# Kernel optimization log

Hardware: AMD Instinct MI355X
Metric: run time of the kernel (lower is better)

## Reference

```python
import jax, jax.numpy as jnp
import numpy as np

N_NODES = 200_000
N_EDGES = 6_400_000
N_GRAPHS = 512


def _graph_conv(x, src, dst, W_rel, b_rel, W_root, n_nodes):
    # PyG GraphConv (aggr='add'): lin_rel(sum_{j->i} x_j) + lin_root(x_i)
    agg = jax.ops.segment_sum(x[src], dst, num_segments=n_nodes)  # [N, in]
    return agg @ W_rel.T + b_rel + x @ W_root.T


def setup_inputs() -> dict:
    key = jax.random.key(0)
    ks = jax.random.split(key, 12)
    x = jax.random.normal(ks[0], (N_NODES, 3), dtype=jnp.float32)
    edge_index = jax.random.randint(ks[1], (2, N_EDGES), 0, N_NODES, dtype=jnp.int64)
    batch = jnp.sort(jax.random.randint(ks[2], (N_NODES,), 0, N_GRAPHS, dtype=jnp.int64))

    def xavier(k, shape):
        fan_out, fan_in = shape
        lim = np.sqrt(6.0 / (fan_in + fan_out)).astype(np.float32)
        return jax.random.uniform(k, shape, jnp.float32, -lim, lim)

    return {
        "x": x, "edge_index": edge_index, "batch": batch,
        "W1_rel": xavier(ks[3], (32, 3)),  "b1": jnp.zeros((32,), jnp.float32), "W1_root": xavier(ks[4], (32, 3)),
        "W2_rel": xavier(ks[5], (16, 32)), "b2": jnp.zeros((16,), jnp.float32), "W2_root": xavier(ks[6], (16, 32)),
        "W3_rel": xavier(ks[7], (8, 16)),  "b3": jnp.zeros((8,), jnp.float32),  "W3_root": xavier(ks[8], (8, 16)),
        "W_lin": xavier(ks[9], (1, 8)),    "b_lin": jnp.zeros((1,), jnp.float32),
    }


def reference(x, edge_index, batch,
              W1_rel, b1, W1_root,
              W2_rel, b2, W2_root,
              W3_rel, b3, W3_root,
              W_lin, b_lin):
    src, dst = edge_index[0], edge_index[1]
    h = jax.nn.relu(_graph_conv(x, src, dst, W1_rel, b1, W1_root, N_NODES))
    h = jax.nn.relu(_graph_conv(h, src, dst, W2_rel, b2, W2_root, N_NODES))
    h = jax.nn.relu(_graph_conv(h, src, dst, W3_rel, b3, W3_root, N_NODES))
    pooled = jax.ops.segment_max(h, batch, num_segments=N_GRAPHS)  # [G, 8]
    out = pooled @ W_lin.T + b_lin  # [G, 1]
    return out[:, 0]
```

## Files before the change

### kernel.cpp

```cpp
#include <hip/hip_runtime.h>
#include <hip/hip_fp16.h>

#define N_NODES 200000
#define N_EDGES 6400000
#define N_GRAPHS 512

#define NB 3125
#define CHUNK 8192
#define NCH 782
#define NGRP 25
#define CPG 32
#define SEG 13
#define SCAP 3072

typedef float vf4 __attribute__((ext_vector_type(4)));
typedef float vf2 __attribute__((ext_vector_type(2)));
typedef unsigned vu2 __attribute__((ext_vector_type(2)));

__device__ __forceinline__ unsigned ntload_u(const unsigned* p) {
  return __builtin_nontemporal_load(p);
}
__device__ __forceinline__ int ntload_i(const int* p) { return __builtin_nontemporal_load(p); }
__device__ __forceinline__ float ntload_f(const float* p) {
  return __builtin_nontemporal_load(p);
}
__device__ __forceinline__ float2 ntload_f2(const float* p) {
  vf2 v = __builtin_nontemporal_load((const vf2*)p);
  return make_float2(v.x, v.y);
}
__device__ __forceinline__ void ntstore_u2(unsigned* p, uint2 v) {
  vu2 t = {v.x, v.y};
  __builtin_nontemporal_store(t, (vu2*)p);
}
__device__ __forceinline__ void ntstore_f2(float* p, float2 v) {
  vf2 t = {v.x, v.y};
  __builtin_nontemporal_store(t, (vf2*)p);
}
__device__ __forceinline__ void ntstore_f4(float* p, float4 v) {
  vf4 t = {v.x, v.y, v.z, v.w};
  __builtin_nontemporal_store(t, (vf4*)p);
}
__device__ __forceinline__ void ntstore_u(unsigned* p, unsigned v) {
  __builtin_nontemporal_store(v, p);
}


__global__ __launch_bounds__(256) void count_kernel(const int* __restrict__ dst,
                                                    unsigned short* __restrict__ H) {
  __shared__ unsigned hist[NB];
  for (int i = threadIdx.x; i < NB; i += 256) hist[i] = 0;
  __syncthreads();
  int c = blockIdx.x;
  long e0 = (long)c * CHUNK;
  long rem = (long)N_EDGES - e0;
  int n = rem > CHUNK ? CHUNK : (int)rem;
  for (int i = threadIdx.x; i < n; i += 256) atomicAdd(&hist[dst[e0 + i] >> 6], 1u);
  __syncthreads();
  for (int i = threadIdx.x; i < NB; i += 256) H[(size_t)c * NB + i] = (unsigned short)hist[i];
}

__global__ __launch_bounds__(256) void scan_bins1_kernel(unsigned short* __restrict__ H,
                                                         unsigned* __restrict__ P) {
  int b = blockIdx.x * 256 + threadIdx.x;
  int g = blockIdx.y;
  if (b >= NB) return;
  int c0 = g * CPG, c1 = min(NCH, (g + 1) * CPG);
  unsigned run = 0;
  for (int c = c0; c < c1; c++) {
    unsigned t = H[(size_t)c * NB + b];
    H[(size_t)c * NB + b] = (unsigned short)run;
    run += t;
  }
  P[(size_t)g * NB + b] = run;
}

__global__ __launch_bounds__(256) void scan_bins2_kernel(unsigned* __restrict__ P,
                                                         unsigned* __restrict__ bucketTotal) {
  int b = blockIdx.x * 256 + threadIdx.x;
  if (b >= NB) return;
  unsigned run = 0;
  for (int g = 0; g < NGRP; g++) {
    unsigned t = P[(size_t)g * NB + b];
    P[(size_t)g * NB + b] = run;
    run += t;
  }
  bucketTotal[b] = run;
}

__global__ __launch_bounds__(256) void scan_total_kernel(const unsigned* __restrict__ bucketTotal,
                                                         unsigned* __restrict__ bucketStart) {
  __shared__ unsigned sv[256 * SEG];
  __shared__ unsigned partial[256];
  int t = threadIdx.x;
  for (int i = t; i < 256 * SEG; i += 256) sv[i] = (i < NB) ? bucketTotal[i] : 0u;
  __syncthreads();
  unsigned sum = 0;
#pragma unroll
  for (int k = 0; k < SEG; k++) sum += sv[t * SEG + k];
  partial[t] = sum;
  __syncthreads();
  for (int off = 1; off < 256; off <<= 1) {
    unsigned add = (t >= off) ? partial[t - off] : 0u;
    __syncthreads();
    partial[t] += add;
    __syncthreads();
  }
  unsigned run = partial[t] - sum;
#pragma unroll
  for (int k = 0; k < SEG; k++) {
    unsigned w = sv[t * SEG + k];
    sv[t * SEG + k] = run;
    run += w;
  }
  __syncthreads();
  for (int i = t; i < NB; i += 256) bucketStart[i] = sv[i];
  if (t == 0) bucketStart[NB] = N_EDGES;
}

__global__ __launch_bounds__(256) void scatter_sorted_kernel(
    const int* __restrict__ src, const int* __restrict__ dst,
    const unsigned short* __restrict__ H, const unsigned* __restrict__ P,
    const unsigned* __restrict__ bucketStart, unsigned* __restrict__ packed) {
  __shared__ unsigned ssort[CHUNK];
  __shared__ unsigned short sbort[CHUNK];
  __shared__ unsigned hist[3328];
  __shared__ unsigned cur[3328];
  __shared__ unsigned partial[256];
  int t = threadIdx.x;
  int c = blockIdx.x;
  int g = c / CPG;
  long e0 = (long)c * CHUNK;
  long rem = (long)N_EDGES - e0;
  int n = rem > CHUNK ? CHUNK : (int)rem;
  for (int i = t; i < 3328; i += 256) hist[i] = 0;
  __syncthreads();
  for (int i = t; i < n; i += 256) atomicAdd(&hist[dst[e0 + i] >> 6], 1u);
  __syncthreads();
  unsigned a[SEG], sum = 0;
#pragma unroll
  for (int k = 0; k < SEG; k++) { a[k] = hist[SEG * t + k]; sum += a[k]; }
  partial[t] = sum;
  __syncthreads();
  for (int off = 1; off < 256; off <<= 1) {
    unsigned add = (t >= off) ? partial[t - off] : 0u;
    __syncthreads();
    partial[t] += add;
    __syncthreads();
  }
  unsigned run = partial[t] - sum;
#pragma unroll
  for (int k = 0; k < SEG; k++) {
    hist[SEG * t + k] = run;
    cur[SEG * t + k] = run;
    run += a[k];
  }
  __syncthreads();
  for (int i = t; i < n; i += 256) {
    int d = dst[e0 + i], s = src[e0 + i];
    int b = d >> 6;
    unsigned r = atomicAdd(&cur[b], 1u);
    ssort[r] = ((unsigned)s << 7) | (unsigned)(d & 63);
    sbort[r] = (unsigned short)b;
  }
  __syncthreads();
  for (int b = t; b < NB; b += 256)
    cur[b] = bucketStart[b] + P[(size_t)g * NB + b] + H[(size_t)c * NB + b] - hist[b];
  __syncthreads();
  for (int j = t; j < n; j += 256) packed[cur[sbort[j]] + j] = ssort[j];
}

__global__ __launch_bounds__(256) void sort2_kernel(const unsigned* __restrict__ packedA,
                                                    const unsigned* __restrict__ bucketStart,
                                                    unsigned* __restrict__ packedB,
                                                    unsigned* __restrict__ nodeStart) {
  __shared__ unsigned buf[SCAP];
  __shared__ unsigned buf2[SCAP];
  __shared__ unsigned hist[64], base[64], cur[64];
  int t = threadIdx.x, b = blockIdx.x;
  unsigned s0 = bucketStart[b], s1 = bucketStart[b + 1];
  int n = (int)(s1 - s0);
  if (t < 64) hist[t] = 0;
  for (int i = t; i < n; i += 256) buf[i] = packedA[s0 + i];
  __syncthreads();
  for (int i = t; i < n; i += 256) atomicAdd(&hist[buf[i] & 63u], 1u);
  __syncthreads();
  if (t == 0) {
    unsigned run = 0;
    for (int k = 0; k < 64; k++) {
      unsigned v = hist[k];
      base[k] = run;
      cur[k] = run;
      run += v;
    }
  }
  __syncthreads();
  if (t < 64) nodeStart[b * 64 + t] = s0 + base[t];
  for (int i = t; i < n; i += 256) {
    unsigned p = buf[i];
    unsigned pos = atomicAdd(&cur[p & 63u], 1u);
    buf2[pos] = p >> 7;
  }
  __syncthreads();
  for (int i = t; i < n; i += 256) packedB[s0 + i] = buf2[i];
  if (b == NB - 1 && t == 0) nodeStart[N_NODES] = N_EDGES;
}

__global__ __launch_bounds__(256) void xpad_kernel(const float* __restrict__ x,
                                                   float4* __restrict__ xp) {
  int n = blockIdx.x * 256 + threadIdx.x;
  if (n >= N_NODES) return;
  xp[n] = make_float4(x[3 * n], x[3 * n + 1], x[3 * n + 2], 0.f);
}

__device__ __forceinline__ void half8_unpack(uint4 g, float* f) {
  const __half2* h2 = reinterpret_cast<const __half2*>(&g);
#pragma unroll
  for (int j = 0; j < 4; j++) {
    float2 fj = __half22float2(h2[j]);
    f[2 * j] = fj.x;
    f[2 * j + 1] = fj.y;
  }
}

__global__ __launch_bounds__(256) void layer1_kernel(
    const unsigned* __restrict__ packed, const unsigned* __restrict__ nodeStart,
    const float4* __restrict__ xp,
    const float* __restrict__ W1_rel, const float* __restrict__ b1,
    const float* __restrict__ W1_root,
    const float* __restrict__ W2_rel, const float* __restrict__ W2_root,
    unsigned* __restrict__ t2h, float* __restrict__ r2) {
  __shared__ float sW1rel[96], sW1root[96], sb1[32], sW2rel[512], sW2root[512];
  __shared__ float plds[256 * 4];
  for (int i = threadIdx.x; i < 96; i += 256) { sW1rel[i] = W1_rel[i]; sW1root[i] = W1_root[i]; }
  for (int i = threadIdx.x; i < 32; i += 256) sb1[i] = b1[i];
  for (int i = threadIdx.x; i < 512; i += 256) { sW2rel[i] = W2_rel[i]; sW2root[i] = W2_root[i]; }
  __syncthreads();
  int t = threadIdx.x, ln = t >> 2, part = t & 3;
  int node = blockIdx.x * 64 + ln;
  unsigned s1v = ntload_u(&nodeStart[node + 1]);
  float a0 = 0.f, a1 = 0.f, a2 = 0.f;
  for (unsigned base = ntload_u(&nodeStart[node]) + part; base < s1v; base += 16) {
    unsigned i1 = base + 4, i2 = base + 8, i3 = base + 12;
    unsigned e0 = ntload_u(&packed[base]);
    unsigned e1 = ntload_u(&packed[i1]);
    unsigned e2 = ntload_u(&packed[i2]);
    unsigned e3 = ntload_u(&packed[i3]);
    float4 g0 = xp[e0], g1 = xp[e1], g2 = xp[e2], g3 = xp[e3];
    float m1 = (i1 < s1v) ? 1.f : 0.f;
    float m2 = (i2 < s1v) ? 1.f : 0.f;
    float m3 = (i3 < s1v) ? 1.f : 0.f;
    a0 += g0.x + m1 * g1.x + m2 * g2.x + m3 * g3.x;
    a1 += g0.y + m1 * g1.y + m2 * g2.y + m3 * g3.y;
    a2 += g0.z + m1 * g1.z + m2 * g2.z + m3 * g3.z;
  }
  plds[t * 4] = a0; plds[t * 4 + 1] = a1; plds[t * 4 + 2] = a2;
  __syncthreads();
  int pb = ln * 16;
  float A0 = plds[pb] + plds[pb + 4] + plds[pb + 8] + plds[pb + 12];
  float A1 = plds[pb + 1] + plds[pb + 5] + plds[pb + 9] + plds[pb + 13];
  float A2 = plds[pb + 2] + plds[pb + 6] + plds[pb + 10] + plds[pb + 14];
  float4 xv = xp[node];
  float h[32];
#pragma unroll
  for (int k = 0; k < 32; k++) {
    float v = sW1rel[3 * k] * A0 + sW1rel[3 * k + 1] * A1 + sW1rel[3 * k + 2] * A2 +
              sW1root[3 * k] * xv.x + sW1root[3 * k + 1] * xv.y + sW1root[3 * k + 2] * xv.z +
              sb1[k];
    h[k] = fmaxf(v, 0.f);
  }
  int jb = part * 4;
  float tv[4], rv[4];
#pragma unroll
  for (int j = 0; j < 4; j++) {
    float acc = 0.f, accr = 0.f;
#pragma unroll
    for (int k = 0; k < 32; k++) {
      acc += sW2rel[32 * (jb + j) + k] * h[k];
      accr += sW2root[32 * (jb + j) + k] * h[k];
    }
    tv[j] = acc;
    rv[j] = accr;
  }
  __half2 p0 = __halves2half2(__float2half_rn(tv[0]), __float2half_rn(tv[1]));
  __half2 p1 = __halves2half2(__float2half_rn(tv[2]), __float2half_rn(tv[3]));
  ntstore_u2(&t2h[(size_t)node * 8 + part * 2], make_uint2(*(unsigned*)&p0, *(unsigned*)&p1));
  ntstore_f4(&r2[(size_t)node * 16 + jb], make_float4(rv[0], rv[1], rv[2], rv[3]));
}

__global__ __launch_bounds__(256) void layer2_kernel(
    const unsigned* __restrict__ packed, const unsigned* __restrict__ nodeStart,
    const uint4* __restrict__ t2h4, const float* __restrict__ r2,
    const float* __restrict__ b2,
    const float* __restrict__ W3_rel, const float* __restrict__ W3_root,
    unsigned* __restrict__ t3h, float* __restrict__ r3) {
  __shared__ float sW3rel[128], sW3root[128], sb2[16];
  __shared__ float plds[256 * 9];
  __shared__ float hlds[32 * 16];
  for (int i = threadIdx.x; i < 128; i += 256) { sW3rel[i] = W3_rel[i]; sW3root[i] = W3_root[i]; }
  if (threadIdx.x < 16) sb2[threadIdx.x] = b2[threadIdx.x];
  __syncthreads();
  int t = threadIdx.x, ln = t >> 3, p = t & 7;
  int node = blockIdx.x * 32 + ln;
  int half = p & 1;
  unsigned s1v = ntload_u(&nodeStart[node + 1]);
  float acc[8];
#pragma unroll
  for (int j = 0; j < 8; j++) acc[j] = 0.f;
  for (unsigned base = ntload_u(&nodeStart[node]) + (p >> 1); base < s1v; base += 16) {
    unsigned i1 = base + 4, i2 = base + 8, i3 = base + 12;
    unsigned e0 = ntload_u(&packed[base]);
    unsigned e1 = ntload_u(&packed[i1]);
    unsigned e2 = ntload_u(&packed[i2]);
    unsigned e3 = ntload_u(&packed[i3]);
    uint4 g0 = t2h4[(size_t)e0 * 2 + half];
    uint4 g1 = t2h4[(size_t)e1 * 2 + half];
    uint4 g2 = t2h4[(size_t)e2 * 2 + half];
    uint4 g3 = t2h4[(size_t)e3 * 2 + half];
    float m1 = (i1 < s1v) ? 1.f : 0.f;
    float m2 = (i2 < s1v) ? 1.f : 0.f;
    float m3 = (i3 < s1v) ? 1.f : 0.f;
    float f0[8], f1[8], f2[8], f3[8];
    half8_unpack(g0, f0);
    half8_unpack(g1, f1);
    half8_unpack(g2, f2);
    half8_unpack(g3, f3);
#pragma unroll
    for (int j = 0; j < 8; j++)
      acc[j] += f0[j] + m1 * f1[j] + m2 * f2[j] + m3 * f3[j];
  }
#pragma unroll
  for (int j = 0; j < 8; j++) plds[t * 9 + j] = acc[j];
  __syncthreads();
  {
    float2 rv = ntload_f2(&r2[(size_t)node * 16 + 2 * p]);
    float hv[2];
#pragma unroll
    for (int k2 = 0; k2 < 2; k2++) {
      int f = 2 * p + k2;
      int fh = f >> 3, fi = f & 7;
      int q0 = (ln * 8 + fh) * 9 + fi;
      float s = plds[q0] + plds[q0 + 18] + plds[q0 + 36] + plds[q0 + 54];
      hv[k2] = s + sb2[f] + (k2 == 0 ? rv.x : rv.y);
    }
    hlds[ln * 16 + 2 * p] = fmaxf(hv[0], 0.f);
    hlds[ln * 16 + 2 * p + 1] = fmaxf(hv[1], 0.f);
  }
  __syncthreads();
  const float* W = (p < 4) ? sW3rel : sW3root;
  int rbase = (p < 4) ? 2 * p : 2 * (p - 4);
  float o0 = 0.f, o1 = 0.f;
#pragma unroll
  for (int k = 0; k < 16; k++) {
    float hv = hlds[ln * 16 + k];
    o0 += W[16 * rbase + k] * hv;
    o1 += W[16 * (rbase + 1) + k] * hv;
  }
  if (p < 4) {
    __half2 pk = __halves2half2(__float2half_rn(o0), __float2half_rn(o1));
    ntstore_u(&t3h[(size_t)node * 4 + p], *(unsigned*)&pk);
  } else {
    ntstore_f2(&r3[(size_t)node * 8 + rbase], make_float2(o0, o1));
  }
}

__global__ __launch_bounds__(256) void layer3_kernel(
    const unsigned* __restrict__ packed, const unsigned* __restrict__ nodeStart,
    const uint4* __restrict__ t3h4, const float* __restrict__ r3,
    const float* __restrict__ b3,
    const int* __restrict__ batch, unsigned* __restrict__ pooled) {
  __shared__ float plds[256 * 9];
  __shared__ float sb3[8];
  __shared__ int sgid[32];
  if (threadIdx.x < 8) sb3[threadIdx.x] = b3[threadIdx.x];
  __syncthreads();
  int t = threadIdx.x, ln = t >> 3, p = t & 7;
  int node = blockIdx.x * 32 + ln;
  unsigned s1v = ntload_u(&nodeStart[node + 1]);
  float acc[8];
#pragma unroll
  for (int j = 0; j < 8; j++) acc[j] = 0.f;
  for (unsigned base = ntload_u(&nodeStart[node]) + p; base < s1v; base += 32) {
    unsigned i1 = base + 8, i2 = base + 16, i3 = base + 24;
    unsigned e0 = ntload_u(&packed[base]);
    unsigned e1 = ntload_u(&packed[i1]);
    unsigned e2 = ntload_u(&packed[i2]);
    unsigned e3 = ntload_u(&packed[i3]);
    uint4 g0 = t3h4[e0];
    uint4 g1 = t3h4[e1];
    uint4 g2 = t3h4[e2];
    uint4 g3 = t3h4[e3];
    float m1 = (i1 < s1v) ? 1.f : 0.f;
    float m2 = (i2 < s1v) ? 1.f : 0.f;
    float m3 = (i3 < s1v) ? 1.f : 0.f;
    float f0[8], f1[8], f2[8], f3[8];
    half8_unpack(g0, f0);
    half8_unpack(g1, f1);
    half8_unpack(g2, f2);
    half8_unpack(g3, f3);
#pragma unroll
    for (int j = 0; j < 8; j++)
      acc[j] += f0[j] + m1 * f1[j] + m2 * f2[j] + m3 * f3[j];
  }
#pragma unroll
  for (int j = 0; j < 8; j++) plds[t * 9 + j] = acc[j];
  __syncthreads();
  int gg = ntload_i(&batch[node]);
  int q0 = ln * 72 + p;
  float v = plds[q0] + plds[q0 + 9] + plds[q0 + 18] + plds[q0 + 27] +
            plds[q0 + 36] + plds[q0 + 45] + plds[q0 + 54] + plds[q0 + 63];
  float h = fmaxf(v + sb3[p] + ntload_f(&r3[(size_t)node * 8 + p]), 0.f);
  __syncthreads();
  plds[ln * 9 + p] = h;
  if (p == 0) sgid[ln] = gg;
  __syncthreads();
  if (t < 8) {
    int gcur = sgid[0];
    float m = plds[t];
    for (int l = 1; l < 32; l++) {
      int g2 = sgid[l];
      float hv = plds[l * 9 + t];
      if (g2 != gcur) {
        atomicMax(&pooled[8 * gcur + t], __float_as_uint(m));
        gcur = g2;
        m = hv;
      } else {
        m = fmaxf(m, hv);
      }
    }
    atomicMax(&pooled[8 * gcur + t], __float_as_uint(m));
  }
}

__global__ __launch_bounds__(256) void final_kernel(
    const unsigned* __restrict__ pooled, const float* __restrict__ W_lin,
    const float* __restrict__ b_lin, float* __restrict__ out) {
  int g = blockIdx.x * blockDim.x + threadIdx.x;
  if (g >= N_GRAPHS) return;
  float acc = b_lin[0];
#pragma unroll
  for (int f = 0; f < 8; f++) acc += __uint_as_float(pooled[8 * g + f]) * W_lin[f];
  out[g] = acc;
}

extern "C" void kernel_launch(void* const* d_in, const int* in_sizes, int n_in,
                              void* d_out, int out_size, void* d_ws, size_t ws_size,
                              hipStream_t stream) {
  const float* x = (const float*)d_in[0];
  const int* ei = (const int*)d_in[1];
  const int* src = ei;
  const int* dst = ei + N_EDGES;
  const int* batch = (const int*)d_in[2];
  const float* W1_rel = (const float*)d_in[3];
  const float* b1 = (const float*)d_in[4];
  const float* W1_root = (const float*)d_in[5];
  const float* W2_rel = (const float*)d_in[6];
  const float* b2 = (const float*)d_in[7];
  const float* W2_root = (const float*)d_in[8];
  const float* W3_rel = (const float*)d_in[9];
  const float* b3 = (const float*)d_in[10];
  const float* W3_root = (const float*)d_in[11];
  const float* W_lin = (const float*)d_in[12];
  const float* b_lin = (const float*)d_in[13];
  float* out = (float*)d_out;

  char* ws = (char*)d_ws;
  unsigned* packedA = (unsigned*)(ws + 0);
  float* r2 = (float*)(ws + 0);
  float* r3 = (float*)(ws + 12800000);
  unsigned* t3h = (unsigned*)(ws + 19200000);
  float4* xpad = (float4*)(ws + 22400000);
  unsigned short* H = (unsigned short*)(ws + 25600000);
  unsigned* packedB = (unsigned*)(ws + 25600000);
  unsigned* t2h = (unsigned*)(ws + 51200128);
  unsigned* pooled = (unsigned*)(ws + 57600128);
  unsigned* bucketStart = (unsigned*)(ws + 57616512);
  unsigned* bucketTotal = (unsigned*)(ws + 57629016);
  unsigned* P = (unsigned*)(ws + 57641516);
  unsigned* nodeStart = (unsigned*)(ws + 57954016);

  hipMemsetAsync(pooled, 0, N_GRAPHS * 8 * sizeof(unsigned), stream);
  hipMemsetAsync(packedB + N_EDGES, 0, 128, stream);

  count_kernel<<<NCH, 256, 0, stream>>>(dst, H);
  scan_bins1_kernel<<<dim3((NB + 255) / 256, NGRP), 256, 0, stream>>>(H, P);
  scan_bins2_kernel<<<(NB + 255) / 256, 256, 0, stream>>>(P, bucketTotal);
  scan_total_kernel<<<1, 256, 0, stream>>>(bucketTotal, bucketStart);
  scatter_sorted_kernel<<<NCH, 256, 0, stream>>>(src, dst, H, P, bucketStart, packedA);
  sort2_kernel<<<NB, 256, 0, stream>>>(packedA, bucketStart, packedB, nodeStart);
  xpad_kernel<<<(N_NODES + 255) / 256, 256, 0, stream>>>(x, xpad);

  layer1_kernel<<<NB, 256, 0, stream>>>(packedB, nodeStart, xpad,
                                        W1_rel, b1, W1_root, W2_rel, W2_root, t2h, r2);
  layer2_kernel<<<N_NODES / 32, 256, 0, stream>>>(packedB, nodeStart, (const uint4*)t2h, r2, b2,
                                                  W3_rel, W3_root, t3h, r3);
  layer3_kernel<<<N_NODES / 32, 256, 0, stream>>>(packedB, nodeStart, (const uint4*)t3h, r3, b3,
                                                  batch, pooled);
  final_kernel<<<(N_GRAPHS + 255) / 256, 256, 0, stream>>>(pooled, W_lin, b_lin, out);
}
```

Baseline: 430.8 us.

## Coarsen first-pass sort buckets to 1024 nodes with per-wave histograms

The two-pass counting sort of edges by destination now uses 196 coarse buckets of 1024 nodes instead of 3125 buckets of 64. This shrinks the histogram, prefix-scan and offset arrays, and the count and scatter kernels keep one privatized histogram per wavefront to cut LDS atomic contention. The second pass uses 512-thread blocks that sort each bucket straight from global memory into its final position. This trades the LDS staging for uncoalesced global scatter writes and far fewer blocks with longer per-block work.

```diff
diff --git a/kernel.cpp b/kernel.cpp
--- a/kernel.cpp
+++ b/kernel.cpp
@@ -5,13 +5,13 @@
 #define N_EDGES 6400000
 #define N_GRAPHS 512
 
-#define NB 3125
+#define NB1 196
+#define CB 1024
 #define CHUNK 8192
 #define NCH 782
 #define NGRP 25
 #define CPG 32
-#define SEG 13
-#define SCAP 3072
+#define ST2 512
 
 typedef float vf4 __attribute__((ext_vector_type(4)));
 typedef float vf2 __attribute__((ext_vector_type(2)));
@@ -47,41 +47,44 @@
 
 __global__ __launch_bounds__(256) void count_kernel(const int* __restrict__ dst,
                                                     unsigned short* __restrict__ H) {
-  __shared__ unsigned hist[NB];
-  for (int i = threadIdx.x; i < NB; i += 256) hist[i] = 0;
+  __shared__ unsigned hist[4][NB1];
+  int t = threadIdx.x, w = t >> 6;
+  for (int i = t; i < 4 * NB1; i += 256) ((unsigned*)hist)[i] = 0;
   __syncthreads();
   int c = blockIdx.x;
   long e0 = (long)c * CHUNK;
   long rem = (long)N_EDGES - e0;
   int n = rem > CHUNK ? CHUNK : (int)rem;
-  for (int i = threadIdx.x; i < n; i += 256) atomicAdd(&hist[dst[e0 + i] >> 6], 1u);
-  __syncthreads();
-  for (int i = threadIdx.x; i < NB; i += 256) H[(size_t)c * NB + i] = (unsigned short)hist[i];
+  for (int i = t; i < n; i += 256) atomicAdd(&hist[w][dst[e0 + i] >> 10], 1u);
+  __syncthreads();
+  for (int b = t; b < NB1; b += 256)
+    H[(size_t)c * NB1 + b] =
+        (unsigned short)(hist[0][b] + hist[1][b] + hist[2][b] + hist[3][b]);
 }
 
 __global__ __launch_bounds__(256) void scan_bins1_kernel(unsigned short* __restrict__ H,
                                                          unsigned* __restrict__ P) {
   int b = blockIdx.x * 256 + threadIdx.x;
   int g = blockIdx.y;
-  if (b >= NB) return;
+  if (b >= NB1) return;
   int c0 = g * CPG, c1 = min(NCH, (g + 1) * CPG);
   unsigned run = 0;
   for (int c = c0; c < c1; c++) {
-    unsigned t = H[(size_t)c * NB + b];
-    H[(size_t)c * NB + b] = (unsigned short)run;
+    unsigned t = H[(size_t)c * NB1 + b];
+    H[(size_t)c * NB1 + b] = (unsigned short)run;
     run += t;
   }
-  P[(size_t)g * NB + b] = run;
+  P[(size_t)g * NB1 + b] = run;
 }
 
 __global__ __launch_bounds__(256) void scan_bins2_kernel(unsigned* __restrict__ P,
                                                          unsigned* __restrict__ bucketTotal) {
   int b = blockIdx.x * 256 + threadIdx.x;
-  if (b >= NB) return;
+  if (b >= NB1) return;
   unsigned run = 0;
   for (int g = 0; g < NGRP; g++) {
-    unsigned t = P[(size_t)g * NB + b];
-    P[(size_t)g * NB + b] = run;
+    unsigned t = P[(size_t)g * NB1 + b];
+    P[(size_t)g * NB1 + b] = run;
     run += t;
   }
   bucketTotal[b] = run;
@@ -89,15 +92,10 @@
 
 __global__ __launch_bounds__(256) void scan_total_kernel(const unsigned* __restrict__ bucketTotal,
                                                          unsigned* __restrict__ bucketStart) {
-  __shared__ unsigned sv[256 * SEG];
   __shared__ unsigned partial[256];
   int t = threadIdx.x;
-  for (int i = t; i < 256 * SEG; i += 256) sv[i] = (i < NB) ? bucketTotal[i] : 0u;
-  __syncthreads();
-  unsigned sum = 0;
-#pragma unroll
-  for (int k = 0; k < SEG; k++) sum += sv[t * SEG + k];
-  partial[t] = sum;
+  unsigned v = (t < NB1) ? bucketTotal[t] : 0u;
+  partial[t] = v;
   __syncthreads();
   for (int off = 1; off < 256; off <<= 1) {
     unsigned add = (t >= off) ? partial[t - off] : 0u;
@@ -105,16 +103,8 @@
     partial[t] += add;
     __syncthreads();
   }
-  unsigned run = partial[t] - sum;
-#pragma unroll
-  for (int k = 0; k < SEG; k++) {
-    unsigned w = sv[t * SEG + k];
-    sv[t * SEG + k] = run;
-    run += w;
-  }
-  __syncthreads();
-  for (int i = t; i < NB; i += 256) bucketStart[i] = sv[i];
-  if (t == 0) bucketStart[NB] = N_EDGES;
+  if (t < NB1) bucketStart[t] = partial[t] - v;
+  if (t == 0) bucketStart[NB1] = N_EDGES;
 }
 
 __global__ __launch_bounds__(256) void scatter_sorted_kernel(
@@ -122,24 +112,27 @@
     const unsigned short* __restrict__ H, const unsigned* __restrict__ P,
     const unsigned* __restrict__ bucketStart, unsigned* __restrict__ packed) {
   __shared__ unsigned ssort[CHUNK];
-  __shared__ unsigned short sbort[CHUNK];
-  __shared__ unsigned hist[3328];
-  __shared__ unsigned cur[3328];
+  __shared__ unsigned char sbort[CHUNK];
+  __shared__ unsigned histw[4][NB1];
+  __shared__ unsigned curw[4][NB1];
+  __shared__ unsigned gbase[NB1];
   __shared__ unsigned partial[256];
-  int t = threadIdx.x;
+  int t = threadIdx.x, w = t >> 6;
   int c = blockIdx.x;
   int g = c / CPG;
   long e0 = (long)c * CHUNK;
   long rem = (long)N_EDGES - e0;
   int n = rem > CHUNK ? CHUNK : (int)rem;
-  for (int i = t; i < 3328; i += 256) hist[i] = 0;
-  __syncthreads();
-  for (int i = t; i < n; i += 256) atomicAdd(&hist[dst[e0 + i] >> 6], 1u);
-  __syncthreads();
-  unsigned a[SEG], sum = 0;
-#pragma unroll
-  for (int k = 0; k < SEG; k++) { a[k] = hist[SEG * t + k]; sum += a[k]; }
-  partial[t] = sum;
+  for (int i = t; i < 4 * NB1; i += 256) ((unsigned*)histw)[i] = 0;
+  __syncthreads();
+  for (int i = t; i < n; i += 256) atomicAdd(&histw[w][dst[e0 + i] >> 10], 1u);
+  __syncthreads();
+  unsigned tot = 0, h0 = 0, h1 = 0, h2 = 0, h3 = 0;
+  if (t < NB1) {
+    h0 = histw[0][t]; h1 = histw[1][t]; h2 = histw[2][t]; h3 = histw[3][t];
+    tot = h0 + h1 + h2 + h3;
+  }
+  partial[t] = tot;
   __syncthreads();
   for (int off = 1; off < 256; off <<= 1) {
     unsigned add = (t >= off) ? partial[t - off] : 0u;
@@ -147,62 +140,68 @@
     partial[t] += add;
     __syncthreads();
   }
-  unsigned run = partial[t] - sum;
-#pragma unroll
-  for (int k = 0; k < SEG; k++) {
-    hist[SEG * t + k] = run;
-    cur[SEG * t + k] = run;
-    run += a[k];
+  if (t < NB1) {
+    unsigned ex = partial[t] - tot;
+    unsigned r = ex;
+    curw[0][t] = r; r += h0;
+    curw[1][t] = r; r += h1;
+    curw[2][t] = r; r += h2;
+    curw[3][t] = r;
+    gbase[t] = bucketStart[t] + P[(size_t)g * NB1 + t] + (unsigned)H[(size_t)c * NB1 + t] - ex;
   }
   __syncthreads();
   for (int i = t; i < n; i += 256) {
     int d = dst[e0 + i], s = src[e0 + i];
-    int b = d >> 6;
-    unsigned r = atomicAdd(&cur[b], 1u);
-    ssort[r] = ((unsigned)s << 7) | (unsigned)(d & 63);
-    sbort[r] = (unsigned short)b;
-  }
-  __syncthreads();
-  for (int b = t; b < NB; b += 256)
-    cur[b] = bucketStart[b] + P[(size_t)g * NB + b] + H[(size_t)c * NB + b] - hist[b];
-  __syncthreads();
-  for (int j = t; j < n; j += 256) packed[cur[sbort[j]] + j] = ssort[j];
-}
-
-__global__ __launch_bounds__(256) void sort2_kernel(const unsigned* __restrict__ packedA,
+    int b = d >> 10;
+    unsigned r = atomicAdd(&curw[w][b], 1u);
+    ssort[r] = ((unsigned)s << 10) | (unsigned)(d & 1023);
+    sbort[r] = (unsigned char)b;
+  }
+  __syncthreads();
+  for (int j = t; j < n; j += 256) packed[gbase[sbort[j]] + j] = ssort[j];
+}
+
+__global__ __launch_bounds__(ST2) void sort2_kernel(const unsigned* __restrict__ packedA,
                                                     const unsigned* __restrict__ bucketStart,
                                                     unsigned* __restrict__ packedB,
                                                     unsigned* __restrict__ nodeStart) {
-  __shared__ unsigned buf[SCAP];
-  __shared__ unsigned buf2[SCAP];
-  __shared__ unsigned hist[64], base[64], cur[64];
+  __shared__ unsigned hist[CB];
+  __shared__ unsigned cur[CB];
+  __shared__ unsigned partial[ST2];
   int t = threadIdx.x, b = blockIdx.x;
   unsigned s0 = bucketStart[b], s1 = bucketStart[b + 1];
   int n = (int)(s1 - s0);
-  if (t < 64) hist[t] = 0;
-  for (int i = t; i < n; i += 256) buf[i] = packedA[s0 + i];
-  __syncthreads();
-  for (int i = t; i < n; i += 256) atomicAdd(&hist[buf[i] & 63u], 1u);
-  __syncthreads();
-  if (t == 0) {
-    unsigned run = 0;
-    for (int k = 0; k < 64; k++) {
-      unsigned v = hist[k];
-      base[k] = run;
-      cur[k] = run;
-      run += v;
-    }
-  }
-  __syncthreads();
-  if (t < 64) nodeStart[b * 64 + t] = s0 + base[t];
-  for (int i = t; i < n; i += 256) {
-    unsigned p = buf[i];
-    unsigned pos = atomicAdd(&cur[p & 63u], 1u);
-    buf2[pos] = p >> 7;
-  }
-  __syncthreads();
-  for (int i = t; i < n; i += 256) packedB[s0 + i] = buf2[i];
-  if (b == NB - 1 && t == 0) nodeStart[N_NODES] = N_EDGES;
+  for (int i = t; i < CB; i += ST2) hist[i] = 0;
+  __syncthreads();
+  for (int i = t; i < n; i += ST2) atomicAdd(&hist[packedA[s0 + i] & 1023u], 1u);
+  __syncthreads();
+  unsigned a0 = hist[2 * t], a1 = hist[2 * t + 1];
+  unsigned sum = a0 + a1;
+  partial[t] = sum;
+  __syncthreads();
+  for (int off = 1; off < ST2; off <<= 1) {
+    unsigned add = (t >= off) ? partial[t - off] : 0u;
+    __syncthreads();
+    partial[t] += add;
+    __syncthreads();
+  }
+  unsigned run = partial[t] - sum;
+  __syncthreads();
+  hist[2 * t] = run;
+  cur[2 * t] = run;
+  hist[2 * t + 1] = run + a0;
+  cur[2 * t + 1] = run + a0;
+  __syncthreads();
+  int gnode = b * CB;
+  for (int k = t; k < CB; k += ST2) {
+    int gn = gnode + k;
+    if (gn <= N_NODES) nodeStart[gn] = s0 + hist[k];
+  }
+  for (int i = t; i < n; i += ST2) {
+    unsigned v = packedA[s0 + i];
+    unsigned pos = atomicAdd(&cur[v & 1023u], 1u);
+    packedB[s0 + pos] = v >> 10;
+  }
 }
 
 __global__ __launch_bounds__(256) void xpad_kernel(const float* __restrict__ x,
@@ -482,15 +481,15 @@
   hipMemsetAsync(packedB + N_EDGES, 0, 128, stream);
 
   count_kernel<<<NCH, 256, 0, stream>>>(dst, H);
-  scan_bins1_kernel<<<dim3((NB + 255) / 256, NGRP), 256, 0, stream>>>(H, P);
-  scan_bins2_kernel<<<(NB + 255) / 256, 256, 0, stream>>>(P, bucketTotal);
+  scan_bins1_kernel<<<dim3((NB1 + 255) / 256, NGRP), 256, 0, stream>>>(H, P);
+  scan_bins2_kernel<<<(NB1 + 255) / 256, 256, 0, stream>>>(P, bucketTotal);
   scan_total_kernel<<<1, 256, 0, stream>>>(bucketTotal, bucketStart);
   scatter_sorted_kernel<<<NCH, 256, 0, stream>>>(src, dst, H, P, bucketStart, packedA);
-  sort2_kernel<<<NB, 256, 0, stream>>>(packedA, bucketStart, packedB, nodeStart);
+  sort2_kernel<<<NB1, ST2, 0, stream>>>(packedA, bucketStart, packedB, nodeStart);
   xpad_kernel<<<(N_NODES + 255) / 256, 256, 0, stream>>>(x, xpad);
 
-  layer1_kernel<<<NB, 256, 0, stream>>>(packedB, nodeStart, xpad,
-                                        W1_rel, b1, W1_root, W2_rel, W2_root, t2h, r2);
+  layer1_kernel<<<N_NODES / 64, 256, 0, stream>>>(packedB, nodeStart, xpad,
+                                                  W1_rel, b1, W1_root, W2_rel, W2_root, t2h, r2);
   layer2_kernel<<<N_NODES / 32, 256, 0, stream>>>(packedB, nodeStart, (const uint4*)t2h, r2, b2,
                                                   W3_rel, W3_root, t3h, r3);
   layer3_kernel<<<N_NODES / 32, 256, 0, stream>>>(packedB, nodeStart, (const uint4*)t3h, r3, b3,
```

After: 442.7 us. 2.7% more time.
